# Performance work log

Hardware: AMD Instinct MI355X
Metric: run time of the kernel (lower is better)

The kernel has to match this reference:

```python
import jax, jax.numpy as jnp
import numpy as np

DIM = 128          # observed dim
LATENT = 128       # SDE state_size
HID = 128          # mu hidden width (hard-coded in source)
BROWNIAN = 2       # brownian_size
N_STEPS = 200      # Euler-Maruyama steps over t in [0, 1]
DT = 1.0 / N_STEPS


def _linear_init(key, fan_in, fan_out):
    # torch nn.Linear default: U(-1/sqrt(fan_in), 1/sqrt(fan_in))
    kw, kb = jax.random.split(key)
    bound = 1.0 / np.sqrt(fan_in)
    w = jax.random.uniform(kw, (fan_in, fan_out), jnp.float32, -bound, bound)
    b = jax.random.uniform(kb, (fan_out,), jnp.float32, -bound, bound)
    return w, b


def setup_inputs() -> dict:
    key = jax.random.key(0)
    ks = jax.random.split(key, 8)
    y = jax.random.normal(ks[0], (32768, DIM), jnp.float32)
    noise = jax.random.normal(ks[1], (N_STEPS, 32768, BROWNIAN), jnp.float32)
    enc_w, enc_b = _linear_init(ks[2], DIM, LATENT)
    mu_w1, mu_b1 = _linear_init(ks[3], LATENT, HID)
    mu_w2, mu_b2 = _linear_init(ks[4], HID, LATENT)
    sig_w, sig_b = _linear_init(ks[5], LATENT, LATENT * BROWNIAN)
    dec_w, dec_b = _linear_init(ks[6], LATENT, DIM)
    return {
        "y": y, "noise": noise,
        "enc_w": enc_w, "enc_b": enc_b,
        "mu_w1": mu_w1, "mu_b1": mu_b1, "mu_w2": mu_w2, "mu_b2": mu_b2,
        "sig_w": sig_w, "sig_b": sig_b,
        "dec_w": dec_w, "dec_b": dec_b,
    }


def reference(y, noise, enc_w, enc_b, mu_w1, mu_b1, mu_w2, mu_b2, sig_w, sig_b, dec_w, dec_b):
    B = y.shape[0]
    # encoder: Linear + exact GELU (torch nn.GELU default)
    z0 = jax.nn.gelu(y @ enc_w + enc_b, approximate=False)

    sqrt_dt = jnp.asarray(np.sqrt(DT), jnp.float32)

    def drift(z):  # f(t, y) = mu(y)
        h = jax.nn.gelu(z @ mu_w1 + mu_b1, approximate=False)
        return h @ mu_w2 + mu_b2

    def diffusion(z):  # g(t, y) -> [B, state, brownian]
        return (z @ sig_w + sig_b).reshape(B, LATENT, BROWNIAN)

    def step(z, xi):
        # Euler-Maruyama (Ito): z += f*dt + g @ dW,  dW = sqrt(dt)*xi
        dW = xi * sqrt_dt                      # [B, K]
        g = diffusion(z)                       # [B, D, K]
        z = z + drift(z) * DT + jnp.einsum("bdk,bk->bd", g, dW)
        return z, None

    zT, _ = jax.lax.scan(step, z0, noise)
    return zT @ dec_w + dec_b
```

## Files before the change

kernel.cpp:

```cpp
#include <hip/hip_runtime.h>
#include <math.h>

#define NSTEPS 200
#define NT     512
#define BR     64
#define SQDT_F 0.07071067811865475f
#define DT_F   0.005f
#define LOSCL  4096.0f
#define LOINV  2.44140625e-4f

typedef float  f32x4 __attribute__((ext_vector_type(4)));
typedef short  s16x8 __attribute__((ext_vector_type(8)));
typedef _Float16 h16x8 __attribute__((ext_vector_type(8)));
typedef unsigned short u16;
typedef unsigned short us4 __attribute__((ext_vector_type(4)));

#define ENC_OFF 0
#define W1_OFF  32768
#define W2_OFF  65536
#define WG0_OFF 98304
#define WG1_OFF 131072
#define DEC_OFF 163840
#define WPK_TOT 196608

__device__ __forceinline__ u16 f2h(float v) {
    _Float16 h = (_Float16)v;
    return __builtin_bit_cast(u16, h);
}
__device__ __forceinline__ float h2f(u16 u) {
    return (float)__builtin_bit_cast(_Float16, u);
}
__device__ __forceinline__ u16 split_hi(float v) { return f2h(v); }
__device__ __forceinline__ u16 split_lo(float v, u16 hi) {
    return f2h((v - h2f(hi)) * LOSCL);
}

__device__ __forceinline__ float gelu_fast(float x) {
    float ax = fabsf(x) * 0.70710678118654752f;
    float t  = __builtin_amdgcn_rcpf(fmaf(0.3275911f, ax, 1.0f));
    float p  = fmaf(t, 1.061405429f, -1.453152027f);
    p = fmaf(t, p, 1.421413741f);
    p = fmaf(t, p, -0.284496736f);
    p = fmaf(t, p, 0.254829592f);
    p = p * t;
    float e  = __expf(-ax * ax);
    float er = fmaf(-p, e, 1.0f);
    er = copysignf(er, x);
    return 0.5f * x * (1.0f + er);
}

__device__ __forceinline__ void mfma16(f32x4& d, s16x8 a, s16x8 b) {
    d = __builtin_amdgcn_mfma_f32_16x16x32_f16(
            __builtin_bit_cast(h16x8, a), __builtin_bit_cast(h16x8, b), d, 0, 0, 0);
}
__device__ __forceinline__ s16x8 ldf(const u16* p) {
    return *reinterpret_cast<const s16x8*>(p);
}

__device__ __forceinline__ int swz(int row) {
    return (row & 7) ^ ((row & 8) >> 2);
}

__global__ void prepack(const float* __restrict__ enc_w, const float* __restrict__ mu_w1,
                        const float* __restrict__ mu_w2, const float* __restrict__ sig_w,
                        const float* __restrict__ dec_w, u16* __restrict__ wpk)
{
    int u = blockIdx.x * 256 + threadIdx.x;
    if (u >= WPK_TOT) return;
    int mat  = u >> 15;
    int r    = u & 32767;
    int i    = r & 7;
    int lane = (r >> 3) & 63;
    int term = (r >> 9) & 1;
    int kc   = (r >> 10) & 3;
    int nt   = (r >> 12) & 7;
    int k = kc * 32 + (lane >> 4) * 8 + i;
    int n = nt * 16 + (lane & 15);
    float v;
    switch (mat) {
        case 0:  v = enc_w[k * 128 + n];         break;
        case 1:  v = mu_w1[k * 128 + n];         break;
        case 2:  v = mu_w2[k * 128 + n];         break;
        case 3:  v = sig_w[k * 256 + 2 * n];     break;
        case 4:  v = sig_w[k * 256 + 2 * n + 1]; break;
        default: v = dec_w[k * 128 + n];         break;
    }
    u16 hi = split_hi(v);
    wpk[u] = term ? split_lo(v, hi) : hi;
}

__global__ __launch_bounds__(NT) void sde_mfma(
    const float* __restrict__ y, const float* __restrict__ noise,
    const float* __restrict__ enc_b, const float* __restrict__ mu_b1,
    const float* __restrict__ mu_b2, const float* __restrict__ sig_b,
    const float* __restrict__ dec_b, const u16* __restrict__ wpk,
    float* __restrict__ out, int Btot)
{
    __shared__ __align__(16) u16 zbh[8192];
    __shared__ __align__(16) u16 zbl[8192];
    __shared__ __align__(16) u16 hbh[8192];
    __shared__ __align__(16) u16 hbl[8192];
    __shared__ float nsb[2][128];

    const int tid  = threadIdx.x;
    const int lane = tid & 63, wid = tid >> 6;
    const int ln   = lane & 15, lg = lane >> 4;
    const size_t brow = (size_t)blockIdx.x * BR;

    const int n0 = wid * 16 + ln;
    const float b10 = mu_b1[n0];
    const float b20 = mu_b2[n0];
    const float bg0 = sig_b[2 * n0];
    const float bg1 = sig_b[2 * n0 + 1];
    const int swzl = swz(ln);

    #pragma unroll
    for (int c = 0; c < 4; c++) {
        int q = c * NT + tid;
        int row = q >> 5, k4 = (q & 31) << 2;
        const float4 v = *reinterpret_cast<const float4*>(y + (brow + row) * 128 + k4);
        int idx = row * 128 + (((k4 >> 3) ^ swz(row)) << 3) + (k4 & 7);
        float vv[4] = {v.x, v.y, v.z, v.w};
        us4 hv, lv;
        #pragma unroll
        for (int e = 0; e < 4; e++) {
            u16 h = split_hi(vv[e]);
            u16 l = split_lo(vv[e], h);
            hv[e] = h; lv[e] = l;
        }
        *reinterpret_cast<us4*>(zbh + idx) = hv;
        *reinterpret_cast<us4*>(zbl + idx) = lv;
    }
    __syncthreads();

    float zr[4][4];

    {
        const float be0 = enc_b[n0];
        f32x4 a0[4], a1[4];
        #pragma unroll
        for (int mt = 0; mt < 4; mt++) {
            a0[mt] = f32x4{be0, be0, be0, be0};
            a1[mt] = f32x4{0, 0, 0, 0};
        }
        #pragma unroll
        for (int kc = 0; kc < 4; kc++) {
            int fo = (((wid << 2) | kc) << 10) + (lane << 3);
            s16x8 bh = ldf(wpk + ENC_OFF + fo);
            s16x8 bl = ldf(wpk + ENC_OFF + fo + 512);
            #pragma unroll
            for (int mt = 0; mt < 4; mt++) {
                int idx = (mt * 16 + ln) * 128 + ((((kc << 2) | lg) ^ swzl) << 3);
                s16x8 ah = ldf(zbh + idx);
                s16x8 al = ldf(zbl + idx);
                mfma16(a0[mt], ah, bh);
                mfma16(a1[mt], al, bh);
                mfma16(a1[mt], ah, bl);
            }
        }
        #pragma unroll
        for (int mt = 0; mt < 4; mt++)
            #pragma unroll
            for (int r = 0; r < 4; r++)
                zr[mt][r] = gelu_fast(fmaf(a1[mt][r], LOINV, a0[mt][r]));
    }
    __syncthreads();

    #pragma unroll
    for (int mt = 0; mt < 4; mt++)
        #pragma unroll
        for (int r = 0; r < 4; r++) {
            int m = 16 * mt + 4 * lg + r;
            int idx = m * 128 + (((n0 >> 3) ^ swz(m)) << 3) + (n0 & 7);
            u16 h = split_hi(zr[mt][r]);
            zbh[idx] = h;
            zbl[idx] = split_lo(zr[mt][r], h);
        }
    if (tid < 128) nsb[0][tid] = noise[brow * 2 + tid];
    __syncthreads();

    const u16* wq = wpk;

    for (int t = 0; t < NSTEPS; t++) {
        asm volatile("" : "+s"(wq));
        {
            int tn = (t + 1 < NSTEPS) ? (t + 1) : t;
            if (tid < 128) nsb[(t + 1) & 1][tid] = noise[((size_t)tn * Btot + brow) * 2 + tid];
        }
        {
            f32x4 a0[4], a1[4];
            #pragma unroll
            for (int mt = 0; mt < 4; mt++) {
                a0[mt] = f32x4{b10, b10, b10, b10};
                a1[mt] = f32x4{0, 0, 0, 0};
            }
            #pragma unroll
            for (int kc = 0; kc < 4; kc++) {
                int fo = (((wid << 2) | kc) << 10) + (lane << 3);
                s16x8 bh = ldf(wq + W1_OFF + fo);
                s16x8 bl = ldf(wq + W1_OFF + fo + 512);
                #pragma unroll
                for (int mt = 0; mt < 4; mt++) {
                    int idx = (mt * 16 + ln) * 128 + ((((kc << 2) | lg) ^ swzl) << 3);
                    s16x8 ah = ldf(zbh + idx);
                    s16x8 al = ldf(zbl + idx);
                    mfma16(a0[mt], ah, bh);
                    mfma16(a1[mt], al, bh);
                    mfma16(a1[mt], ah, bl);
                }
            }
            #pragma unroll
            for (int mt = 0; mt < 4; mt++)
                #pragma unroll
                for (int r = 0; r < 4; r++) {
                    float hv = gelu_fast(fmaf(a1[mt][r], LOINV, a0[mt][r]));
                    int m = 16 * mt + 4 * lg + r;
                    int idx = m * 128 + (((n0 >> 3) ^ swz(m)) << 3) + (n0 & 7);
                    u16 h = split_hi(hv);
                    hbh[idx] = h;
                    hbl[idx] = split_lo(hv, h);
                }
        }
        {
            f32x4 q0h[4], q0l[4], q1h[4], q1l[4];
            #pragma unroll
            for (int mt = 0; mt < 4; mt++) {
                q0h[mt] = f32x4{bg0, bg0, bg0, bg0}; q0l[mt] = f32x4{0, 0, 0, 0};
                q1h[mt] = f32x4{bg1, bg1, bg1, bg1}; q1l[mt] = f32x4{0, 0, 0, 0};
            }
            #pragma unroll 2
            for (int kc = 0; kc < 4; kc++) {
                int fo = (((wid << 2) | kc) << 10) + (lane << 3);
                s16x8 b0h = ldf(wq + WG0_OFF + fo);
                s16x8 b0l = ldf(wq + WG0_OFF + fo + 512);
                s16x8 b1h = ldf(wq + WG1_OFF + fo);
                s16x8 b1l = ldf(wq + WG1_OFF + fo + 512);
                #pragma unroll
                for (int mt = 0; mt < 4; mt++) {
                    int idx = (mt * 16 + ln) * 128 + ((((kc << 2) | lg) ^ swzl) << 3);
                    s16x8 ah = ldf(zbh + idx);
                    s16x8 al = ldf(zbl + idx);
                    mfma16(q0h[mt], ah, b0h);
                    mfma16(q0l[mt], al, b0h);
                    mfma16(q0l[mt], ah, b0l);
                    mfma16(q1h[mt], ah, b1h);
                    mfma16(q1l[mt], al, b1h);
                    mfma16(q1l[mt], ah, b1l);
                }
            }
            const float* np = nsb[t & 1];
            #pragma unroll
            for (int mt = 0; mt < 4; mt++)
                #pragma unroll
                for (int r = 0; r < 4; r++) {
                    int m = 16 * mt + 4 * lg + r;
                    float dw0 = np[2 * m] * SQDT_F;
                    float dw1 = np[2 * m + 1] * SQDT_F;
                    float gv0 = fmaf(q0l[mt][r], LOINV, q0h[mt][r]);
                    float gv1 = fmaf(q1l[mt][r], LOINV, q1h[mt][r]);
                    zr[mt][r] = fmaf(gv0, dw0, fmaf(gv1, dw1, zr[mt][r]));
                }
        }
        __syncthreads();

        {
            f32x4 a0[4], a1[4];
            #pragma unroll
            for (int mt = 0; mt < 4; mt++) {
                a0[mt] = f32x4{b20, b20, b20, b20};
                a1[mt] = f32x4{0, 0, 0, 0};
            }
            #pragma unroll
            for (int kc = 0; kc < 4; kc++) {
                int fo = (((wid << 2) | kc) << 10) + (lane << 3);
                s16x8 bh = ldf(wq + W2_OFF + fo);
                s16x8 bl = ldf(wq + W2_OFF + fo + 512);
                #pragma unroll
                for (int mt = 0; mt < 4; mt++) {
                    int idx = (mt * 16 + ln) * 128 + ((((kc << 2) | lg) ^ swzl) << 3);
                    s16x8 ah = ldf(hbh + idx);
                    s16x8 al = ldf(hbl + idx);
                    mfma16(a0[mt], ah, bh);
                    mfma16(a1[mt], al, bh);
                    mfma16(a1[mt], ah, bl);
                }
            }
            #pragma unroll
            for (int mt = 0; mt < 4; mt++)
                #pragma unroll
                for (int r = 0; r < 4; r++) {
                    float drift = fmaf(a1[mt][r], LOINV, a0[mt][r]);
                    float v = fmaf(drift, DT_F, zr[mt][r]);
                    zr[mt][r] = v;
                    int m = 16 * mt + 4 * lg + r;
                    int idx = m * 128 + (((n0 >> 3) ^ swz(m)) << 3) + (n0 & 7);
                    u16 h = split_hi(v);
                    zbh[idx] = h;
                    zbl[idx] = split_lo(v, h);
                }
        }
        __syncthreads();
    }

    {
        const float bd0 = dec_b[n0];
        f32x4 a0[4], a1[4];
        #pragma unroll
        for (int mt = 0; mt < 4; mt++) {
            a0[mt] = f32x4{bd0, bd0, bd0, bd0};
            a1[mt] = f32x4{0, 0, 0, 0};
        }
        #pragma unroll
        for (int kc = 0; kc < 4; kc++) {
            int fo = (((wid << 2) | kc) << 10) + (lane << 3);
            s16x8 bh = ldf(wpk + DEC_OFF + fo);
            s16x8 bl = ldf(wpk + DEC_OFF + fo + 512);
            #pragma unroll
            for (int mt = 0; mt < 4; mt++) {
                int idx = (mt * 16 + ln) * 128 + ((((kc << 2) | lg) ^ swzl) << 3);
                s16x8 ah = ldf(zbh + idx);
                s16x8 al = ldf(zbl + idx);
                mfma16(a0[mt], ah, bh);
                mfma16(a1[mt], al, bh);
                mfma16(a1[mt], ah, bl);
            }
        }
        #pragma unroll
        for (int mt = 0; mt < 4; mt++)
            #pragma unroll
            for (int r = 0; r < 4; r++) {
                int m = 16 * mt + 4 * lg + r;
                out[(brow + m) * 128 + n0] = fmaf(a1[mt][r], LOINV, a0[mt][r]);
            }
    }
}

extern "C" void kernel_launch(void* const* d_in, const int* in_sizes, int n_in,
                              void* d_out, int out_size, void* d_ws, size_t ws_size,
                              hipStream_t stream) {
    const float* y     = (const float*)d_in[0];
    const float* noise = (const float*)d_in[1];
    const float* enc_w = (const float*)d_in[2];
    const float* enc_b = (const float*)d_in[3];
    const float* mu_w1 = (const float*)d_in[4];
    const float* mu_b1 = (const float*)d_in[5];
    const float* mu_w2 = (const float*)d_in[6];
    const float* mu_b2 = (const float*)d_in[7];
    const float* sig_w = (const float*)d_in[8];
    const float* sig_b = (const float*)d_in[9];
    const float* dec_w = (const float*)d_in[10];
    const float* dec_b = (const float*)d_in[11];
    float* out = (float*)d_out;
    u16* wpk = (u16*)d_ws;

    const int Btot = in_sizes[0] / 128;
    prepack<<<(WPK_TOT + 255) / 256, 256, 0, stream>>>(enc_w, mu_w1, mu_w2, sig_w, dec_w, wpk);
    sde_mfma<<<Btot / BR, NT, 0, stream>>>(y, noise, enc_b, mu_b1, mu_b2, sig_b, dec_b,
                                           wpk, out, Btot);
}
```

Baseline: 2.877 ms.

## Transpose MFMA roles so weights are A operand, shrink block to 16 rows

Restructures the SDE kernel so each block handles 16 batch rows with 256 threads instead of 64 rows with 512. Weights become the MFMA A operand and activations the B operand, with a new k-permuted prepack. Each wave owns two output 16-column tiles, and activations pass through small register-fragment-shaped LDS buffers (double-buffered z) rather than swizzled full-row tiles. The aim is more blocks for better occupancy and latency hiding, and less LDS traffic per step, at the cost of reloading weight fragments from global/L2 for four times as many blocks.

```diff
diff --git a/kernel.cpp b/kernel.cpp
--- a/kernel.cpp
+++ b/kernel.cpp
@@ -2,8 +2,8 @@
 #include <math.h>
 
 #define NSTEPS 200
-#define NT     512
-#define BR     64
+#define NT     256
+#define BR     16
 #define SQDT_F 0.07071067811865475f
 #define DT_F   0.005f
 #define LOSCL  4096.0f
@@ -13,7 +13,6 @@
 typedef short  s16x8 __attribute__((ext_vector_type(8)));
 typedef _Float16 h16x8 __attribute__((ext_vector_type(8)));
 typedef unsigned short u16;
-typedef unsigned short us4 __attribute__((ext_vector_type(4)));
 
 #define ENC_OFF 0
 #define W1_OFF  32768
@@ -55,10 +54,6 @@
 }
 __device__ __forceinline__ s16x8 ldf(const u16* p) {
     return *reinterpret_cast<const s16x8*>(p);
-}
-
-__device__ __forceinline__ int swz(int row) {
-    return (row & 7) ^ ((row & 8) >> 2);
 }
 
 __global__ void prepack(const float* __restrict__ enc_w, const float* __restrict__ mu_w1,
@@ -74,7 +69,7 @@
     int term = (r >> 9) & 1;
     int kc   = (r >> 10) & 3;
     int nt   = (r >> 12) & 7;
-    int k = kc * 32 + (lane >> 4) * 8 + i;
+    int k = kc * 32 + 16 * (i >> 2) + 4 * (lane >> 4) + (i & 3);
     int n = nt * 16 + (lane & 15);
     float v;
     switch (mat) {
@@ -96,87 +91,66 @@
     const float* __restrict__ dec_b, const u16* __restrict__ wpk,
     float* __restrict__ out, int Btot)
 {
-    __shared__ __align__(16) u16 zbh[8192];
-    __shared__ __align__(16) u16 zbl[8192];
-    __shared__ __align__(16) u16 hbh[8192];
-    __shared__ __align__(16) u16 hbl[8192];
-    __shared__ float nsb[2][128];
+    __shared__ __align__(16) u16 zx[2][4][2][512];
+    __shared__ __align__(16) u16 hx[4][2][512];
+    __shared__ float bb[4][128];
+    __shared__ float nsb[2][32];
 
     const int tid  = threadIdx.x;
     const int lane = tid & 63, wid = tid >> 6;
     const int ln   = lane & 15, lg = lane >> 4;
     const size_t brow = (size_t)blockIdx.x * BR;
 
-    const int n0 = wid * 16 + ln;
-    const float b10 = mu_b1[n0];
-    const float b20 = mu_b2[n0];
-    const float bg0 = sig_b[2 * n0];
-    const float bg1 = sig_b[2 * n0 + 1];
-    const int swzl = swz(ln);
-
-    #pragma unroll
-    for (int c = 0; c < 4; c++) {
-        int q = c * NT + tid;
-        int row = q >> 5, k4 = (q & 31) << 2;
-        const float4 v = *reinterpret_cast<const float4*>(y + (brow + row) * 128 + k4);
-        int idx = row * 128 + (((k4 >> 3) ^ swz(row)) << 3) + (k4 & 7);
-        float vv[4] = {v.x, v.y, v.z, v.w};
-        us4 hv, lv;
-        #pragma unroll
-        for (int e = 0; e < 4; e++) {
-            u16 h = split_hi(vv[e]);
-            u16 l = split_lo(vv[e], h);
-            hv[e] = h; lv[e] = l;
-        }
-        *reinterpret_cast<us4*>(zbh + idx) = hv;
-        *reinterpret_cast<us4*>(zbl + idx) = lv;
-    }
-    __syncthreads();
-
-    float zr[4][4];
+    if (tid < 128) {
+        bb[0][tid] = mu_b1[tid];
+        bb[1][tid] = mu_b2[tid];
+        bb[2][tid] = sig_b[2 * tid];
+        bb[3][tid] = sig_b[2 * tid + 1];
+    }
+    if (tid < 32) nsb[0][tid] = noise[(brow + (tid >> 1)) * 2 + (tid & 1)];
+    volatile const float (*bbv)[128] = (volatile const float (*)[128])bb;
+
+    float zm[2][4];
 
     {
-        const float be0 = enc_b[n0];
-        f32x4 a0[4], a1[4];
-        #pragma unroll
-        for (int mt = 0; mt < 4; mt++) {
-            a0[mt] = f32x4{be0, be0, be0, be0};
-            a1[mt] = f32x4{0, 0, 0, 0};
-        }
+        s16x8 yfh[4], yfl[4];
         #pragma unroll
         for (int kc = 0; kc < 4; kc++) {
-            int fo = (((wid << 2) | kc) << 10) + (lane << 3);
-            s16x8 bh = ldf(wpk + ENC_OFF + fo);
-            s16x8 bl = ldf(wpk + ENC_OFF + fo + 512);
-            #pragma unroll
-            for (int mt = 0; mt < 4; mt++) {
-                int idx = (mt * 16 + ln) * 128 + ((((kc << 2) | lg) ^ swzl) << 3);
-                s16x8 ah = ldf(zbh + idx);
-                s16x8 al = ldf(zbl + idx);
-                mfma16(a0[mt], ah, bh);
-                mfma16(a1[mt], al, bh);
-                mfma16(a1[mt], ah, bl);
-            }
-        }
-        #pragma unroll
-        for (int mt = 0; mt < 4; mt++)
+            float vv[8];
+            #pragma unroll
+            for (int s = 0; s < 2; s++) {
+                const float4 v = *reinterpret_cast<const float4*>(
+                    y + (brow + ln) * 128 + kc * 32 + 16 * s + 4 * lg);
+                vv[4*s+0] = v.x; vv[4*s+1] = v.y; vv[4*s+2] = v.z; vv[4*s+3] = v.w;
+            }
+            s16x8 th, tl;
+            #pragma unroll
+            for (int e = 0; e < 8; e++) {
+                u16 hh = split_hi(vv[e]);
+                th[e] = (short)hh;
+                tl[e] = (short)split_lo(vv[e], hh);
+            }
+            yfh[kc] = th; yfl[kc] = tl;
+        }
+        #pragma unroll
+        for (int s = 0; s < 2; s++) {
+            const int jt = 2 * wid + s;
+            f32x4 a0, a1;
+            #pragma unroll
+            for (int r = 0; r < 4; r++) { a0[r] = enc_b[16 * jt + 4 * lg + r]; a1[r] = 0.0f; }
+            #pragma unroll
+            for (int kc = 0; kc < 4; kc++) {
+                const u16* ap = wpk + ENC_OFF + ((jt * 4 + kc) * 2) * 512 + lane * 8;
+                s16x8 wh = ldf(ap), wl = ldf(ap + 512);
+                mfma16(a0, wh, yfh[kc]);
+                mfma16(a1, wl, yfh[kc]);
+                mfma16(a1, wh, yfl[kc]);
+            }
             #pragma unroll
             for (int r = 0; r < 4; r++)
-                zr[mt][r] = gelu_fast(fmaf(a1[mt][r], LOINV, a0[mt][r]));
-    }
-    __syncthreads();
-
-    #pragma unroll
-    for (int mt = 0; mt < 4; mt++)
-        #pragma unroll
-        for (int r = 0; r < 4; r++) {
-            int m = 16 * mt + 4 * lg + r;
-            int idx = m * 128 + (((n0 >> 3) ^ swz(m)) << 3) + (n0 & 7);
-            u16 h = split_hi(zr[mt][r]);
-            zbh[idx] = h;
-            zbl[idx] = split_lo(zr[mt][r], h);
-        }
-    if (tid < 128) nsb[0][tid] = noise[brow * 2 + tid];
+                zm[s][r] = gelu_fast(fmaf(a1[r], LOINV, a0[r]));
+        }
+    }
     __syncthreads();
 
     const u16* wq = wpk;
@@ -185,153 +159,163 @@
         asm volatile("" : "+s"(wq));
         {
             int tn = (t + 1 < NSTEPS) ? (t + 1) : t;
-            if (tid < 128) nsb[(t + 1) & 1][tid] = noise[((size_t)tn * Btot + brow) * 2 + tid];
-        }
-        {
-            f32x4 a0[4], a1[4];
-            #pragma unroll
-            for (int mt = 0; mt < 4; mt++) {
-                a0[mt] = f32x4{b10, b10, b10, b10};
-                a1[mt] = f32x4{0, 0, 0, 0};
-            }
+            if (tid < 32)
+                nsb[(t + 1) & 1][tid] = noise[((size_t)tn * Btot + brow + (tid >> 1)) * 2 + (tid & 1)];
+        }
+        {
+            s16x8 th, tl;
+            #pragma unroll
+            for (int e = 0; e < 8; e++) {
+                float v = zm[e >> 2][e & 3];
+                u16 hh = split_hi(v);
+                th[e] = (short)hh;
+                tl[e] = (short)split_lo(v, hh);
+            }
+            *reinterpret_cast<s16x8*>(&zx[t & 1][wid][0][lane * 8]) = th;
+            *reinterpret_cast<s16x8*>(&zx[t & 1][wid][1][lane * 8]) = tl;
+        }
+        __syncthreads();
+
+        s16x8 zfh[4], zfl[4];
+        #pragma unroll
+        for (int kc = 0; kc < 4; kc++) {
+            zfh[kc] = ldf(&zx[t & 1][kc][0][lane * 8]);
+            zfl[kc] = ldf(&zx[t & 1][kc][1][lane * 8]);
+        }
+
+        float hvv[2][4];
+        #pragma unroll
+        for (int s = 0; s < 2; s++) {
+            const int jt = 2 * wid + s;
+            f32x4 a0, a1;
+            #pragma unroll
+            for (int r = 0; r < 4; r++) { a0[r] = bbv[0][16 * jt + 4 * lg + r]; a1[r] = 0.0f; }
             #pragma unroll
             for (int kc = 0; kc < 4; kc++) {
-                int fo = (((wid << 2) | kc) << 10) + (lane << 3);
-                s16x8 bh = ldf(wq + W1_OFF + fo);
-                s16x8 bl = ldf(wq + W1_OFF + fo + 512);
-                #pragma unroll
-                for (int mt = 0; mt < 4; mt++) {
-                    int idx = (mt * 16 + ln) * 128 + ((((kc << 2) | lg) ^ swzl) << 3);
-                    s16x8 ah = ldf(zbh + idx);
-                    s16x8 al = ldf(zbl + idx);
-                    mfma16(a0[mt], ah, bh);
-                    mfma16(a1[mt], al, bh);
-                    mfma16(a1[mt], ah, bl);
+                const u16* ap = wq + W1_OFF + ((jt * 4 + kc) * 2) * 512 + lane * 8;
+                s16x8 wh = ldf(ap), wl = ldf(ap + 512);
+                mfma16(a0, wh, zfh[kc]);
+                mfma16(a1, wl, zfh[kc]);
+                mfma16(a1, wh, zfl[kc]);
+            }
+            #pragma unroll
+            for (int r = 0; r < 4; r++)
+                hvv[s][r] = gelu_fast(fmaf(a1[r], LOINV, a0[r]));
+        }
+        {
+            s16x8 th, tl;
+            #pragma unroll
+            for (int e = 0; e < 8; e++) {
+                float v = hvv[e >> 2][e & 3];
+                u16 hh = split_hi(v);
+                th[e] = (short)hh;
+                tl[e] = (short)split_lo(v, hh);
+            }
+            *reinterpret_cast<s16x8*>(&hx[wid][0][lane * 8]) = th;
+            *reinterpret_cast<s16x8*>(&hx[wid][1][lane * 8]) = tl;
+        }
+
+        {
+            const float dw0 = nsb[t & 1][2 * ln] * SQDT_F;
+            const float dw1 = nsb[t & 1][2 * ln + 1] * SQDT_F;
+            #pragma unroll
+            for (int s = 0; s < 2; s++) {
+                const int nt = 2 * wid + s;
+                f32x4 q0h, q0l, q1h, q1l;
+                #pragma unroll
+                for (int r = 0; r < 4; r++) {
+                    q0h[r] = bbv[2][16 * nt + 4 * lg + r]; q0l[r] = 0.0f;
+                    q1h[r] = bbv[3][16 * nt + 4 * lg + r]; q1l[r] = 0.0f;
                 }
-            }
-            #pragma unroll
-            for (int mt = 0; mt < 4; mt++)
+                #pragma unroll
+                for (int kc = 0; kc < 4; kc++) {
+                    const u16* p0 = wq + WG0_OFF + ((nt * 4 + kc) * 2) * 512 + lane * 8;
+                    const u16* p1 = wq + WG1_OFF + ((nt * 4 + kc) * 2) * 512 + lane * 8;
+                    s16x8 w0h = ldf(p0), w0l = ldf(p0 + 512);
+                    s16x8 w1h = ldf(p1), w1l = ldf(p1 + 512);
+                    mfma16(q0h, w0h, zfh[kc]);
+                    mfma16(q0l, w0l, zfh[kc]);
+                    mfma16(q0l, w0h, zfl[kc]);
+                    mfma16(q1h, w1h, zfh[kc]);
+                    mfma16(q1l, w1l, zfh[kc]);
+                    mfma16(q1l, w1h, zfl[kc]);
+                }
                 #pragma unroll
                 for (int r = 0; r < 4; r++) {
-                    float hv = gelu_fast(fmaf(a1[mt][r], LOINV, a0[mt][r]));
-                    int m = 16 * mt + 4 * lg + r;
-                    int idx = m * 128 + (((n0 >> 3) ^ swz(m)) << 3) + (n0 & 7);
-                    u16 h = split_hi(hv);
-                    hbh[idx] = h;
-                    hbl[idx] = split_lo(hv, h);
+                    float gv0 = fmaf(q0l[r], LOINV, q0h[r]);
+                    float gv1 = fmaf(q1l[r], LOINV, q1h[r]);
+                    zm[s][r] = fmaf(gv0, dw0, fmaf(gv1, dw1, zm[s][r]));
                 }
-        }
-        {
-            f32x4 q0h[4], q0l[4], q1h[4], q1l[4];
-            #pragma unroll
-            for (int mt = 0; mt < 4; mt++) {
-                q0h[mt] = f32x4{bg0, bg0, bg0, bg0}; q0l[mt] = f32x4{0, 0, 0, 0};
-                q1h[mt] = f32x4{bg1, bg1, bg1, bg1}; q1l[mt] = f32x4{0, 0, 0, 0};
-            }
-            #pragma unroll 2
+            }
+        }
+        __syncthreads();
+
+        {
+            s16x8 hfh[4], hfl[4];
+            #pragma unroll
             for (int kc = 0; kc < 4; kc++) {
-                int fo = (((wid << 2) | kc) << 10) + (lane << 3);
-                s16x8 b0h = ldf(wq + WG0_OFF + fo);
-                s16x8 b0l = ldf(wq + WG0_OFF + fo + 512);
-                s16x8 b1h = ldf(wq + WG1_OFF + fo);
-                s16x8 b1l = ldf(wq + WG1_OFF + fo + 512);
-                #pragma unroll
-                for (int mt = 0; mt < 4; mt++) {
-                    int idx = (mt * 16 + ln) * 128 + ((((kc << 2) | lg) ^ swzl) << 3);
-                    s16x8 ah = ldf(zbh + idx);
-                    s16x8 al = ldf(zbl + idx);
-                    mfma16(q0h[mt], ah, b0h);
-                    mfma16(q0l[mt], al, b0h);
-                    mfma16(q0l[mt], ah, b0l);
-                    mfma16(q1h[mt], ah, b1h);
-                    mfma16(q1l[mt], al, b1h);
-                    mfma16(q1l[mt], ah, b1l);
+                hfh[kc] = ldf(&hx[kc][0][lane * 8]);
+                hfl[kc] = ldf(&hx[kc][1][lane * 8]);
+            }
+            #pragma unroll
+            for (int s = 0; s < 2; s++) {
+                const int nt = 2 * wid + s;
+                f32x4 a0, a1;
+                #pragma unroll
+                for (int r = 0; r < 4; r++) { a0[r] = bbv[1][16 * nt + 4 * lg + r]; a1[r] = 0.0f; }
+                #pragma unroll
+                for (int kc = 0; kc < 4; kc++) {
+                    const u16* ap = wq + W2_OFF + ((nt * 4 + kc) * 2) * 512 + lane * 8;
+                    s16x8 wh = ldf(ap), wl = ldf(ap + 512);
+                    mfma16(a0, wh, hfh[kc]);
+                    mfma16(a1, wl, hfh[kc]);
+                    mfma16(a1, wh, hfl[kc]);
                 }
-            }
-            const float* np = nsb[t & 1];
-            #pragma unroll
-            for (int mt = 0; mt < 4; mt++)
-                #pragma unroll
-                for (int r = 0; r < 4; r++) {
-                    int m = 16 * mt + 4 * lg + r;
-                    float dw0 = np[2 * m] * SQDT_F;
-                    float dw1 = np[2 * m + 1] * SQDT_F;
-                    float gv0 = fmaf(q0l[mt][r], LOINV, q0h[mt][r]);
-                    float gv1 = fmaf(q1l[mt][r], LOINV, q1h[mt][r]);
-                    zr[mt][r] = fmaf(gv0, dw0, fmaf(gv1, dw1, zr[mt][r]));
-                }
-        }
-        __syncthreads();
-
-        {
-            f32x4 a0[4], a1[4];
-            #pragma unroll
-            for (int mt = 0; mt < 4; mt++) {
-                a0[mt] = f32x4{b20, b20, b20, b20};
-                a1[mt] = f32x4{0, 0, 0, 0};
-            }
+                #pragma unroll
+                for (int r = 0; r < 4; r++)
+                    zm[s][r] = fmaf(fmaf(a1[r], LOINV, a0[r]), DT_F, zm[s][r]);
+            }
+        }
+    }
+
+    {
+        s16x8 th, tl;
+        #pragma unroll
+        for (int e = 0; e < 8; e++) {
+            float v = zm[e >> 2][e & 3];
+            u16 hh = split_hi(v);
+            th[e] = (short)hh;
+            tl[e] = (short)split_lo(v, hh);
+        }
+        *reinterpret_cast<s16x8*>(&zx[0][wid][0][lane * 8]) = th;
+        *reinterpret_cast<s16x8*>(&zx[0][wid][1][lane * 8]) = tl;
+    }
+    __syncthreads();
+    {
+        s16x8 zfh[4], zfl[4];
+        #pragma unroll
+        for (int kc = 0; kc < 4; kc++) {
+            zfh[kc] = ldf(&zx[0][kc][0][lane * 8]);
+            zfl[kc] = ldf(&zx[0][kc][1][lane * 8]);
+        }
+        #pragma unroll
+        for (int s = 0; s < 2; s++) {
+            const int nt = 2 * wid + s;
+            f32x4 a0, a1;
+            #pragma unroll
+            for (int r = 0; r < 4; r++) { a0[r] = dec_b[16 * nt + 4 * lg + r]; a1[r] = 0.0f; }
             #pragma unroll
             for (int kc = 0; kc < 4; kc++) {
-                int fo = (((wid << 2) | kc) << 10) + (lane << 3);
-                s16x8 bh = ldf(wq + W2_OFF + fo);
-                s16x8 bl = ldf(wq + W2_OFF + fo + 512);
-                #pragma unroll
-                for (int mt = 0; mt < 4; mt++) {
-                    int idx = (mt * 16 + ln) * 128 + ((((kc << 2) | lg) ^ swzl) << 3);
-                    s16x8 ah = ldf(hbh + idx);
-                    s16x8 al = ldf(hbl + idx);
-                    mfma16(a0[mt], ah, bh);
-                    mfma16(a1[mt], al, bh);
-                    mfma16(a1[mt], ah, bl);
-                }
-            }
-            #pragma unroll
-            for (int mt = 0; mt < 4; mt++)
-                #pragma unroll
-                for (int r = 0; r < 4; r++) {
-                    float drift = fmaf(a1[mt][r], LOINV, a0[mt][r]);
-                    float v = fmaf(drift, DT_F, zr[mt][r]);
-                    zr[mt][r] = v;
-                    int m = 16 * mt + 4 * lg + r;
-                    int idx = m * 128 + (((n0 >> 3) ^ swz(m)) << 3) + (n0 & 7);
-                    u16 h = split_hi(v);
-                    zbh[idx] = h;
-                    zbl[idx] = split_lo(v, h);
-                }
-        }
-        __syncthreads();
-    }
-
-    {
-        const float bd0 = dec_b[n0];
-        f32x4 a0[4], a1[4];
-        #pragma unroll
-        for (int mt = 0; mt < 4; mt++) {
-            a0[mt] = f32x4{bd0, bd0, bd0, bd0};
-            a1[mt] = f32x4{0, 0, 0, 0};
-        }
-        #pragma unroll
-        for (int kc = 0; kc < 4; kc++) {
-            int fo = (((wid << 2) | kc) << 10) + (lane << 3);
-            s16x8 bh = ldf(wpk + DEC_OFF + fo);
-            s16x8 bl = ldf(wpk + DEC_OFF + fo + 512);
-            #pragma unroll
-            for (int mt = 0; mt < 4; mt++) {
-                int idx = (mt * 16 + ln) * 128 + ((((kc << 2) | lg) ^ swzl) << 3);
-                s16x8 ah = ldf(zbh + idx);
-                s16x8 al = ldf(zbl + idx);
-                mfma16(a0[mt], ah, bh);
-                mfma16(a1[mt], al, bh);
-                mfma16(a1[mt], ah, bl);
-            }
-        }
-        #pragma unroll
-        for (int mt = 0; mt < 4; mt++)
-            #pragma unroll
-            for (int r = 0; r < 4; r++) {
-                int m = 16 * mt + 4 * lg + r;
-                out[(brow + m) * 128 + n0] = fmaf(a1[mt][r], LOINV, a0[mt][r]);
-            }
+                const u16* ap = wpk + DEC_OFF + ((nt * 4 + kc) * 2) * 512 + lane * 8;
+                s16x8 wh = ldf(ap), wl = ldf(ap + 512);
+                mfma16(a0, wh, zfh[kc]);
+                mfma16(a1, wl, zfh[kc]);
+                mfma16(a1, wh, zfl[kc]);
+            }
+            #pragma unroll
+            for (int r = 0; r < 4; r++)
+                out[(brow + ln) * 128 + 16 * nt + 4 * lg + r] = fmaf(a1[r], LOINV, a0[r]);
+        }
     }
 }
 
```

New measurement: 5.220 ms. 81.5% more time.

## Pack two independent 64-row groups into one 1024-thread block

Applied to the files above, without the earlier changes.

Each block now runs two independent 512-thread halves, each handling its own 64 batch rows with separate LDS buffers, so a block covers 128 rows and the grid is halved. Both halves share __syncthreads, which could let weight fetches from global/L2 be shared or cached across the pair and changes how waves are scheduled per CU. The cost is twice the LDS per block (about 128KB) and block-wide barriers that couple two independent problems, which may limit occupancy and add barrier stalls.

```diff
diff --git a/kernel.cpp b/kernel.cpp
--- a/kernel.cpp
+++ b/kernel.cpp
@@ -2,8 +2,8 @@
 #include <math.h>
 
 #define NSTEPS 200
-#define NT     512
-#define BR     64
+#define NT     1024
+#define BRB    128
 #define SQDT_F 0.07071067811865475f
 #define DT_F   0.005f
 #define LOSCL  4096.0f
@@ -96,16 +96,18 @@
     const float* __restrict__ dec_b, const u16* __restrict__ wpk,
     float* __restrict__ out, int Btot)
 {
-    __shared__ __align__(16) u16 zbh[8192];
-    __shared__ __align__(16) u16 zbl[8192];
-    __shared__ __align__(16) u16 hbh[8192];
-    __shared__ __align__(16) u16 hbl[8192];
-    __shared__ float nsb[2][128];
+    __shared__ __align__(16) u16 zbh[2][8192];
+    __shared__ __align__(16) u16 zbl[2][8192];
+    __shared__ __align__(16) u16 hbh[2][8192];
+    __shared__ __align__(16) u16 hbl[2][8192];
+    __shared__ float nsb[2][2][128];
 
     const int tid  = threadIdx.x;
-    const int lane = tid & 63, wid = tid >> 6;
+    const int pid  = tid >> 9;
+    const int ptid = tid & 511;
+    const int lane = ptid & 63, wid = ptid >> 6;
     const int ln   = lane & 15, lg = lane >> 4;
-    const size_t brow = (size_t)blockIdx.x * BR;
+    const size_t brow = (size_t)blockIdx.x * BRB + (size_t)pid * 64;
 
     const int n0 = wid * 16 + ln;
     const float b10 = mu_b1[n0];
@@ -116,7 +118,7 @@
 
     #pragma unroll
     for (int c = 0; c < 4; c++) {
-        int q = c * NT + tid;
+        int q = c * 512 + ptid;
         int row = q >> 5, k4 = (q & 31) << 2;
         const float4 v = *reinterpret_cast<const float4*>(y + (brow + row) * 128 + k4);
         int idx = row * 128 + (((k4 >> 3) ^ swz(row)) << 3) + (k4 & 7);
@@ -128,8 +130,8 @@
             u16 l = split_lo(vv[e], h);
             hv[e] = h; lv[e] = l;
         }
-        *reinterpret_cast<us4*>(zbh + idx) = hv;
-        *reinterpret_cast<us4*>(zbl + idx) = lv;
+        *reinterpret_cast<us4*>(&zbh[pid][idx]) = hv;
+        *reinterpret_cast<us4*>(&zbl[pid][idx]) = lv;
     }
     __syncthreads();
 
@@ -151,8 +153,8 @@
             #pragma unroll
             for (int mt = 0; mt < 4; mt++) {
                 int idx = (mt * 16 + ln) * 128 + ((((kc << 2) | lg) ^ swzl) << 3);
-                s16x8 ah = ldf(zbh + idx);
-                s16x8 al = ldf(zbl + idx);
+                s16x8 ah = ldf(&zbh[pid][idx]);
+                s16x8 al = ldf(&zbl[pid][idx]);
                 mfma16(a0[mt], ah, bh);
                 mfma16(a1[mt], al, bh);
                 mfma16(a1[mt], ah, bl);
@@ -173,10 +175,10 @@
             int m = 16 * mt + 4 * lg + r;
             int idx = m * 128 + (((n0 >> 3) ^ swz(m)) << 3) + (n0 & 7);
             u16 h = split_hi(zr[mt][r]);
-            zbh[idx] = h;
-            zbl[idx] = split_lo(zr[mt][r], h);
-        }
-    if (tid < 128) nsb[0][tid] = noise[brow * 2 + tid];
+            zbh[pid][idx] = h;
+            zbl[pid][idx] = split_lo(zr[mt][r], h);
+        }
+    if (ptid < 128) nsb[pid][0][ptid] = noise[brow * 2 + ptid];
     __syncthreads();
 
     const u16* wq = wpk;
@@ -185,7 +187,7 @@
         asm volatile("" : "+s"(wq));
         {
             int tn = (t + 1 < NSTEPS) ? (t + 1) : t;
-            if (tid < 128) nsb[(t + 1) & 1][tid] = noise[((size_t)tn * Btot + brow) * 2 + tid];
+            if (ptid < 128) nsb[pid][(t + 1) & 1][ptid] = noise[((size_t)tn * Btot + brow) * 2 + ptid];
         }
         {
             f32x4 a0[4], a1[4];
@@ -202,8 +204,8 @@
                 #pragma unroll
                 for (int mt = 0; mt < 4; mt++) {
                     int idx = (mt * 16 + ln) * 128 + ((((kc << 2) | lg) ^ swzl) << 3);
-                    s16x8 ah = ldf(zbh + idx);
-                    s16x8 al = ldf(zbl + idx);
+                    s16x8 ah = ldf(&zbh[pid][idx]);
+                    s16x8 al = ldf(&zbl[pid][idx]);
                     mfma16(a0[mt], ah, bh);
                     mfma16(a1[mt], al, bh);
                     mfma16(a1[mt], ah, bl);
@@ -217,8 +219,8 @@
                     int m = 16 * mt + 4 * lg + r;
                     int idx = m * 128 + (((n0 >> 3) ^ swz(m)) << 3) + (n0 & 7);
                     u16 h = split_hi(hv);
-                    hbh[idx] = h;
-                    hbl[idx] = split_lo(hv, h);
+                    hbh[pid][idx] = h;
+                    hbl[pid][idx] = split_lo(hv, h);
                 }
         }
         {
@@ -238,8 +240,8 @@
                 #pragma unroll
                 for (int mt = 0; mt < 4; mt++) {
                     int idx = (mt * 16 + ln) * 128 + ((((kc << 2) | lg) ^ swzl) << 3);
-                    s16x8 ah = ldf(zbh + idx);
-                    s16x8 al = ldf(zbl + idx);
+                    s16x8 ah = ldf(&zbh[pid][idx]);
+                    s16x8 al = ldf(&zbl[pid][idx]);
                     mfma16(q0h[mt], ah, b0h);
                     mfma16(q0l[mt], al, b0h);
                     mfma16(q0l[mt], ah, b0l);
@@ -248,7 +250,7 @@
                     mfma16(q1l[mt], ah, b1l);
                 }
             }
-            const float* np = nsb[t & 1];
+            const float* np = nsb[pid][t & 1];
             #pragma unroll
             for (int mt = 0; mt < 4; mt++)
                 #pragma unroll
@@ -278,8 +280,8 @@
                 #pragma unroll
                 for (int mt = 0; mt < 4; mt++) {
                     int idx = (mt * 16 + ln) * 128 + ((((kc << 2) | lg) ^ swzl) << 3);
-                    s16x8 ah = ldf(hbh + idx);
-                    s16x8 al = ldf(hbl + idx);
+                    s16x8 ah = ldf(&hbh[pid][idx]);
+                    s16x8 al = ldf(&hbl[pid][idx]);
                     mfma16(a0[mt], ah, bh);
                     mfma16(a1[mt], al, bh);
                     mfma16(a1[mt], ah, bl);
@@ -295,8 +297,8 @@
                     int m = 16 * mt + 4 * lg + r;
                     int idx = m * 128 + (((n0 >> 3) ^ swz(m)) << 3) + (n0 & 7);
                     u16 h = split_hi(v);
-                    zbh[idx] = h;
-                    zbl[idx] = split_lo(v, h);
+                    zbh[pid][idx] = h;
+                    zbl[pid][idx] = split_lo(v, h);
                 }
         }
         __syncthreads();
@@ -318,8 +320,8 @@
             #pragma unroll
             for (int mt = 0; mt < 4; mt++) {
                 int idx = (mt * 16 + ln) * 128 + ((((kc << 2) | lg) ^ swzl) << 3);
-                s16x8 ah = ldf(zbh + idx);
-                s16x8 al = ldf(zbl + idx);
+                s16x8 ah = ldf(&zbh[pid][idx]);
+                s16x8 al = ldf(&zbl[pid][idx]);
                 mfma16(a0[mt], ah, bh);
                 mfma16(a1[mt], al, bh);
                 mfma16(a1[mt], ah, bl);
@@ -355,6 +357,6 @@
 
     const int Btot = in_sizes[0] / 128;
     prepack<<<(WPK_TOT + 255) / 256, 256, 0, stream>>>(enc_w, mu_w1, mu_w2, sig_w, dec_w, wpk);
-    sde_mfma<<<Btot / BR, NT, 0, stream>>>(y, noise, enc_b, mu_b1, mu_b2, sig_b, dec_b,
-                                           wpk, out, Btot);
-}
+    sde_mfma<<<Btot / BRB, NT, 0, stream>>>(y, noise, enc_b, mu_b1, mu_b2, sig_b, dec_b,
+                                            wpk, out, Btot);
+}
```

Result: slower. 5.469 ms (+90.1%).

## Transpose MFMA operand roles and repack activations into fragment-native LDS layout

Applied to the files above, without the earlier changes.

Swaps the MFMA operands so weights act as the A operand and activations as B, producing outputs where each lane holds four consecutive features of one row. Activations are stored in LDS in the exact fragment order the MFMA reads, with hi/lo halves interleaved, replacing the XOR-swizzled row-major layout and scalar 16-bit stores with vectorized 4-element stores. The weight prepack permutes the k index to match. Biases move to shared memory read through volatile loads, the output store becomes a float4 write, and noise is indexed per row. This is meant to cut LDS store instructions and address arithmetic, at the cost of possible new bank conflicts and extra LDS bias reads.

```diff
diff --git a/kernel.cpp b/kernel.cpp
--- a/kernel.cpp
+++ b/kernel.cpp
@@ -22,6 +22,8 @@
 #define WG1_OFF 131072
 #define DEC_OFF 163840
 #define WPK_TOT 196608
+
+#define FO(kc, mt, term) (((((kc) * 4 + (mt)) * 2) + (term)) * 512)
 
 __device__ __forceinline__ u16 f2h(float v) {
     _Float16 h = (_Float16)v;
@@ -55,10 +57,6 @@
 }
 __device__ __forceinline__ s16x8 ldf(const u16* p) {
     return *reinterpret_cast<const s16x8*>(p);
-}
-
-__device__ __forceinline__ int swz(int row) {
-    return (row & 7) ^ ((row & 8) >> 2);
 }
 
 __global__ void prepack(const float* __restrict__ enc_w, const float* __restrict__ mu_w1,
@@ -74,7 +72,7 @@
     int term = (r >> 9) & 1;
     int kc   = (r >> 10) & 3;
     int nt   = (r >> 12) & 7;
-    int k = kc * 32 + (lane >> 4) * 8 + i;
+    int k = kc * 32 + 16 * (i >> 2) + 4 * (lane >> 4) + (i & 3);
     int n = nt * 16 + (lane & 15);
     float v;
     switch (mat) {
@@ -96,86 +94,86 @@
     const float* __restrict__ dec_b, const u16* __restrict__ wpk,
     float* __restrict__ out, int Btot)
 {
-    __shared__ __align__(16) u16 zbh[8192];
-    __shared__ __align__(16) u16 zbl[8192];
-    __shared__ __align__(16) u16 hbh[8192];
-    __shared__ __align__(16) u16 hbl[8192];
+    __shared__ __align__(16) u16 zx[16384];
+    __shared__ __align__(16) u16 hx[16384];
+    __shared__ float bb[4][128];
     __shared__ float nsb[2][128];
 
     const int tid  = threadIdx.x;
-    const int lane = tid & 63, wid = tid >> 6;
+    const int lane = tid & 63, jt = tid >> 6;
     const int ln   = lane & 15, lg = lane >> 4;
     const size_t brow = (size_t)blockIdx.x * BR;
 
-    const int n0 = wid * 16 + ln;
-    const float b10 = mu_b1[n0];
-    const float b20 = mu_b2[n0];
-    const float bg0 = sig_b[2 * n0];
-    const float bg1 = sig_b[2 * n0 + 1];
-    const int swzl = swz(ln);
+    const int jb  = 16 * jt + 4 * lg;
+    const int pub = FO(jt >> 1, 0, 0) + lane * 8 + 4 * (jt & 1);
+
+    if (tid < 128)      bb[0][tid]       = mu_b1[tid];
+    else if (tid < 256) bb[1][tid - 128] = mu_b2[tid - 128];
+    else if (tid < 384) bb[2][tid - 256] = sig_b[2 * (tid - 256)];
+    else                bb[3][tid - 384] = sig_b[2 * (tid - 384) + 1];
+    volatile const float* vb = &bb[0][0];
 
     #pragma unroll
-    for (int c = 0; c < 4; c++) {
-        int q = c * NT + tid;
-        int row = q >> 5, k4 = (q & 31) << 2;
-        const float4 v = *reinterpret_cast<const float4*>(y + (brow + row) * 128 + k4);
-        int idx = row * 128 + (((k4 >> 3) ^ swz(row)) << 3) + (k4 & 7);
+    for (int cc = 0; cc < 4; cc++) {
+        int q = cc * NT + tid;
+        int m = q >> 5, cq = (q & 31) << 2;
+        const float4 v = *reinterpret_cast<const float4*>(y + (brow + m) * 128 + cq);
+        int kc = cq >> 5, a = (cq >> 4) & 1, b = (cq >> 2) & 3;
+        int ad = FO(kc, m >> 4, 0) + ((m & 15) + 16 * b) * 8 + 4 * a;
         float vv[4] = {v.x, v.y, v.z, v.w};
         us4 hv, lv;
         #pragma unroll
         for (int e = 0; e < 4; e++) {
             u16 h = split_hi(vv[e]);
-            u16 l = split_lo(vv[e], h);
-            hv[e] = h; lv[e] = l;
-        }
-        *reinterpret_cast<us4*>(zbh + idx) = hv;
-        *reinterpret_cast<us4*>(zbl + idx) = lv;
+            hv[e] = h; lv[e] = split_lo(vv[e], h);
+        }
+        *reinterpret_cast<us4*>(zx + ad)       = hv;
+        *reinterpret_cast<us4*>(zx + ad + 512) = lv;
     }
     __syncthreads();
 
-    float zr[4][4];
+    float zm[4][4];
 
     {
-        const float be0 = enc_b[n0];
+        f32x4 eb;
+        #pragma unroll
+        for (int r = 0; r < 4; r++) eb[r] = enc_b[jb + r];
         f32x4 a0[4], a1[4];
         #pragma unroll
-        for (int mt = 0; mt < 4; mt++) {
-            a0[mt] = f32x4{be0, be0, be0, be0};
-            a1[mt] = f32x4{0, 0, 0, 0};
-        }
-        #pragma unroll
+        for (int mt = 0; mt < 4; mt++) { a0[mt] = eb; a1[mt] = f32x4{0, 0, 0, 0}; }
+        #pragma unroll 2
         for (int kc = 0; kc < 4; kc++) {
-            int fo = (((wid << 2) | kc) << 10) + (lane << 3);
-            s16x8 bh = ldf(wpk + ENC_OFF + fo);
-            s16x8 bl = ldf(wpk + ENC_OFF + fo + 512);
-            #pragma unroll
-            for (int mt = 0; mt < 4; mt++) {
-                int idx = (mt * 16 + ln) * 128 + ((((kc << 2) | lg) ^ swzl) << 3);
-                s16x8 ah = ldf(zbh + idx);
-                s16x8 al = ldf(zbl + idx);
-                mfma16(a0[mt], ah, bh);
-                mfma16(a1[mt], al, bh);
-                mfma16(a1[mt], ah, bl);
+            const u16* ap = wpk + ENC_OFF + ((jt * 4 + kc) * 2) * 512 + lane * 8;
+            s16x8 wh = ldf(ap), wl = ldf(ap + 512);
+            #pragma unroll
+            for (int mt = 0; mt < 4; mt++) {
+                int zo = FO(kc, mt, 0) + lane * 8;
+                s16x8 zh_ = ldf(zx + zo), zl_ = ldf(zx + zo + 512);
+                mfma16(a0[mt], wh, zh_);
+                mfma16(a1[mt], wl, zh_);
+                mfma16(a1[mt], wh, zl_);
             }
         }
         #pragma unroll
         for (int mt = 0; mt < 4; mt++)
             #pragma unroll
             for (int r = 0; r < 4; r++)
-                zr[mt][r] = gelu_fast(fmaf(a1[mt][r], LOINV, a0[mt][r]));
+                zm[mt][r] = gelu_fast(fmaf(a1[mt][r], LOINV, a0[mt][r]));
     }
     __syncthreads();
 
     #pragma unroll
-    for (int mt = 0; mt < 4; mt++)
+    for (int mt = 0; mt < 4; mt++) {
+        us4 hv, lv;
         #pragma unroll
         for (int r = 0; r < 4; r++) {
-            int m = 16 * mt + 4 * lg + r;
-            int idx = m * 128 + (((n0 >> 3) ^ swz(m)) << 3) + (n0 & 7);
-            u16 h = split_hi(zr[mt][r]);
-            zbh[idx] = h;
-            zbl[idx] = split_lo(zr[mt][r], h);
-        }
+            u16 h = split_hi(zm[mt][r]);
+            hv[r] = h; lv[r] = split_lo(zm[mt][r], h);
+        }
+        int ad = pub + mt * 1024;
+        *reinterpret_cast<us4*>(zx + ad)       = hv;
+        *reinterpret_cast<us4*>(zx + ad + 512) = lv;
+    }
     if (tid < 128) nsb[0][tid] = noise[brow * 2 + tid];
     __syncthreads();
 
@@ -188,150 +186,152 @@
             if (tid < 128) nsb[(t + 1) & 1][tid] = noise[((size_t)tn * Btot + brow) * 2 + tid];
         }
         {
+            f32x4 b1v;
+            #pragma unroll
+            for (int r = 0; r < 4; r++) b1v[r] = vb[0 * 128 + jb + r];
             f32x4 a0[4], a1[4];
             #pragma unroll
-            for (int mt = 0; mt < 4; mt++) {
-                a0[mt] = f32x4{b10, b10, b10, b10};
-                a1[mt] = f32x4{0, 0, 0, 0};
-            }
-            #pragma unroll
-            for (int kc = 0; kc < 4; kc++) {
-                int fo = (((wid << 2) | kc) << 10) + (lane << 3);
-                s16x8 bh = ldf(wq + W1_OFF + fo);
-                s16x8 bl = ldf(wq + W1_OFF + fo + 512);
-                #pragma unroll
-                for (int mt = 0; mt < 4; mt++) {
-                    int idx = (mt * 16 + ln) * 128 + ((((kc << 2) | lg) ^ swzl) << 3);
-                    s16x8 ah = ldf(zbh + idx);
-                    s16x8 al = ldf(zbl + idx);
-                    mfma16(a0[mt], ah, bh);
-                    mfma16(a1[mt], al, bh);
-                    mfma16(a1[mt], ah, bl);
-                }
-            }
-            #pragma unroll
-            for (int mt = 0; mt < 4; mt++)
-                #pragma unroll
-                for (int r = 0; r < 4; r++) {
-                    float hv = gelu_fast(fmaf(a1[mt][r], LOINV, a0[mt][r]));
-                    int m = 16 * mt + 4 * lg + r;
-                    int idx = m * 128 + (((n0 >> 3) ^ swz(m)) << 3) + (n0 & 7);
-                    u16 h = split_hi(hv);
-                    hbh[idx] = h;
-                    hbl[idx] = split_lo(hv, h);
-                }
-        }
-        {
-            f32x4 q0h[4], q0l[4], q1h[4], q1l[4];
-            #pragma unroll
-            for (int mt = 0; mt < 4; mt++) {
-                q0h[mt] = f32x4{bg0, bg0, bg0, bg0}; q0l[mt] = f32x4{0, 0, 0, 0};
-                q1h[mt] = f32x4{bg1, bg1, bg1, bg1}; q1l[mt] = f32x4{0, 0, 0, 0};
-            }
+            for (int mt = 0; mt < 4; mt++) { a0[mt] = b1v; a1[mt] = f32x4{0, 0, 0, 0}; }
             #pragma unroll 2
             for (int kc = 0; kc < 4; kc++) {
-                int fo = (((wid << 2) | kc) << 10) + (lane << 3);
-                s16x8 b0h = ldf(wq + WG0_OFF + fo);
-                s16x8 b0l = ldf(wq + WG0_OFF + fo + 512);
-                s16x8 b1h = ldf(wq + WG1_OFF + fo);
-                s16x8 b1l = ldf(wq + WG1_OFF + fo + 512);
+                const u16* ap = wq + W1_OFF + ((jt * 4 + kc) * 2) * 512 + lane * 8;
+                s16x8 wh = ldf(ap), wl = ldf(ap + 512);
                 #pragma unroll
                 for (int mt = 0; mt < 4; mt++) {
-                    int idx = (mt * 16 + ln) * 128 + ((((kc << 2) | lg) ^ swzl) << 3);
-                    s16x8 ah = ldf(zbh + idx);
-                    s16x8 al = ldf(zbl + idx);
-                    mfma16(q0h[mt], ah, b0h);
-                    mfma16(q0l[mt], al, b0h);
-                    mfma16(q0l[mt], ah, b0l);
-                    mfma16(q1h[mt], ah, b1h);
-                    mfma16(q1l[mt], al, b1h);
-                    mfma16(q1l[mt], ah, b1l);
+                    int zo = FO(kc, mt, 0) + lane * 8;
+                    s16x8 zh_ = ldf(zx + zo), zl_ = ldf(zx + zo + 512);
+                    mfma16(a0[mt], wh, zh_);
+                    mfma16(a1[mt], wl, zh_);
+                    mfma16(a1[mt], wh, zl_);
+                }
+            }
+            #pragma unroll
+            for (int mt = 0; mt < 4; mt++) {
+                us4 hv, lv;
+                #pragma unroll
+                for (int r = 0; r < 4; r++) {
+                    float h = gelu_fast(fmaf(a1[mt][r], LOINV, a0[mt][r]));
+                    u16 hh = split_hi(h);
+                    hv[r] = hh; lv[r] = split_lo(h, hh);
+                }
+                int ad = pub + mt * 1024;
+                *reinterpret_cast<us4*>(hx + ad)       = hv;
+                *reinterpret_cast<us4*>(hx + ad + 512) = lv;
+            }
+        }
+        {
+            f32x4 g0v, g1v;
+            #pragma unroll
+            for (int r = 0; r < 4; r++) {
+                g0v[r] = vb[2 * 128 + jb + r];
+                g1v[r] = vb[3 * 128 + jb + r];
+            }
+            f32x4 q0h[4], q0l[4], q1h[4], q1l[4];
+            #pragma unroll
+            for (int mt = 0; mt < 4; mt++) {
+                q0h[mt] = g0v; q0l[mt] = f32x4{0, 0, 0, 0};
+                q1h[mt] = g1v; q1l[mt] = f32x4{0, 0, 0, 0};
+            }
+            #pragma unroll 2
+            for (int kc = 0; kc < 4; kc++) {
+                const u16* p0 = wq + WG0_OFF + ((jt * 4 + kc) * 2) * 512 + lane * 8;
+                const u16* p1 = wq + WG1_OFF + ((jt * 4 + kc) * 2) * 512 + lane * 8;
+                s16x8 w0h = ldf(p0), w0l = ldf(p0 + 512);
+                s16x8 w1h = ldf(p1), w1l = ldf(p1 + 512);
+                #pragma unroll
+                for (int mt = 0; mt < 4; mt++) {
+                    int zo = FO(kc, mt, 0) + lane * 8;
+                    s16x8 zh_ = ldf(zx + zo), zl_ = ldf(zx + zo + 512);
+                    mfma16(q0h[mt], w0h, zh_);
+                    mfma16(q0l[mt], w0l, zh_);
+                    mfma16(q0l[mt], w0h, zl_);
+                    mfma16(q1h[mt], w1h, zh_);
+                    mfma16(q1l[mt], w1l, zh_);
+                    mfma16(q1l[mt], w1h, zl_);
                 }
             }
             const float* np = nsb[t & 1];
             #pragma unroll
-            for (int mt = 0; mt < 4; mt++)
+            for (int mt = 0; mt < 4; mt++) {
+                int mrow = ln + 16 * mt;
+                float dw0 = np[2 * mrow] * SQDT_F;
+                float dw1 = np[2 * mrow + 1] * SQDT_F;
                 #pragma unroll
                 for (int r = 0; r < 4; r++) {
-                    int m = 16 * mt + 4 * lg + r;
-                    float dw0 = np[2 * m] * SQDT_F;
-                    float dw1 = np[2 * m + 1] * SQDT_F;
                     float gv0 = fmaf(q0l[mt][r], LOINV, q0h[mt][r]);
                     float gv1 = fmaf(q1l[mt][r], LOINV, q1h[mt][r]);
-                    zr[mt][r] = fmaf(gv0, dw0, fmaf(gv1, dw1, zr[mt][r]));
-                }
+                    zm[mt][r] = fmaf(gv0, dw0, fmaf(gv1, dw1, zm[mt][r]));
+                }
+            }
         }
         __syncthreads();
 
         {
+            f32x4 b2v;
+            #pragma unroll
+            for (int r = 0; r < 4; r++) b2v[r] = vb[1 * 128 + jb + r];
             f32x4 a0[4], a1[4];
             #pragma unroll
-            for (int mt = 0; mt < 4; mt++) {
-                a0[mt] = f32x4{b20, b20, b20, b20};
-                a1[mt] = f32x4{0, 0, 0, 0};
-            }
-            #pragma unroll
+            for (int mt = 0; mt < 4; mt++) { a0[mt] = b2v; a1[mt] = f32x4{0, 0, 0, 0}; }
+            #pragma unroll 2
             for (int kc = 0; kc < 4; kc++) {
-                int fo = (((wid << 2) | kc) << 10) + (lane << 3);
-                s16x8 bh = ldf(wq + W2_OFF + fo);
-                s16x8 bl = ldf(wq + W2_OFF + fo + 512);
+                const u16* ap = wq + W2_OFF + ((jt * 4 + kc) * 2) * 512 + lane * 8;
+                s16x8 wh = ldf(ap), wl = ldf(ap + 512);
                 #pragma unroll
                 for (int mt = 0; mt < 4; mt++) {
-                    int idx = (mt * 16 + ln) * 128 + ((((kc << 2) | lg) ^ swzl) << 3);
-                    s16x8 ah = ldf(hbh + idx);
-                    s16x8 al = ldf(hbl + idx);
-                    mfma16(a0[mt], ah, bh);
-                    mfma16(a1[mt], al, bh);
-                    mfma16(a1[mt], ah, bl);
-                }
-            }
-            #pragma unroll
-            for (int mt = 0; mt < 4; mt++)
+                    int ho = FO(kc, mt, 0) + lane * 8;
+                    s16x8 hh_ = ldf(hx + ho), hl_ = ldf(hx + ho + 512);
+                    mfma16(a0[mt], wh, hh_);
+                    mfma16(a1[mt], wl, hh_);
+                    mfma16(a1[mt], wh, hl_);
+                }
+            }
+            #pragma unroll
+            for (int mt = 0; mt < 4; mt++) {
+                us4 hv, lv;
                 #pragma unroll
                 for (int r = 0; r < 4; r++) {
                     float drift = fmaf(a1[mt][r], LOINV, a0[mt][r]);
-                    float v = fmaf(drift, DT_F, zr[mt][r]);
-                    zr[mt][r] = v;
-                    int m = 16 * mt + 4 * lg + r;
-                    int idx = m * 128 + (((n0 >> 3) ^ swz(m)) << 3) + (n0 & 7);
-                    u16 h = split_hi(v);
-                    zbh[idx] = h;
-                    zbl[idx] = split_lo(v, h);
-                }
+                    float v = fmaf(drift, DT_F, zm[mt][r]);
+                    zm[mt][r] = v;
+                    u16 hh = split_hi(v);
+                    hv[r] = hh; lv[r] = split_lo(v, hh);
+                }
+                int ad = pub + mt * 1024;
+                *reinterpret_cast<us4*>(zx + ad)       = hv;
+                *reinterpret_cast<us4*>(zx + ad + 512) = lv;
+            }
         }
         __syncthreads();
     }
 
     {
-        const float bd0 = dec_b[n0];
+        f32x4 dbv;
+        #pragma unroll
+        for (int r = 0; r < 4; r++) dbv[r] = dec_b[jb + r];
         f32x4 a0[4], a1[4];
         #pragma unroll
+        for (int mt = 0; mt < 4; mt++) { a0[mt] = dbv; a1[mt] = f32x4{0, 0, 0, 0}; }
+        #pragma unroll 2
+        for (int kc = 0; kc < 4; kc++) {
+            const u16* ap = wpk + DEC_OFF + ((jt * 4 + kc) * 2) * 512 + lane * 8;
+            s16x8 wh = ldf(ap), wl = ldf(ap + 512);
+            #pragma unroll
+            for (int mt = 0; mt < 4; mt++) {
+                int zo = FO(kc, mt, 0) + lane * 8;
+                s16x8 zh_ = ldf(zx + zo), zl_ = ldf(zx + zo + 512);
+                mfma16(a0[mt], wh, zh_);
+                mfma16(a1[mt], wl, zh_);
+                mfma16(a1[mt], wh, zl_);
+            }
+        }
+        #pragma unroll
         for (int mt = 0; mt < 4; mt++) {
-            a0[mt] = f32x4{bd0, bd0, bd0, bd0};
-            a1[mt] = f32x4{0, 0, 0, 0};
-        }
-        #pragma unroll
-        for (int kc = 0; kc < 4; kc++) {
-            int fo = (((wid << 2) | kc) << 10) + (lane << 3);
-            s16x8 bh = ldf(wpk + DEC_OFF + fo);
-            s16x8 bl = ldf(wpk + DEC_OFF + fo + 512);
-            #pragma unroll
-            for (int mt = 0; mt < 4; mt++) {
-                int idx = (mt * 16 + ln) * 128 + ((((kc << 2) | lg) ^ swzl) << 3);
-                s16x8 ah = ldf(zbh + idx);
-                s16x8 al = ldf(zbl + idx);
-                mfma16(a0[mt], ah, bh);
-                mfma16(a1[mt], al, bh);
-                mfma16(a1[mt], ah, bl);
-            }
-        }
-        #pragma unroll
-        for (int mt = 0; mt < 4; mt++)
-            #pragma unroll
-            for (int r = 0; r < 4; r++) {
-                int m = 16 * mt + 4 * lg + r;
-                out[(brow + m) * 128 + n0] = fmaf(a1[mt][r], LOINV, a0[mt][r]);
-            }
+            f32x4 o;
+            #pragma unroll
+            for (int r = 0; r < 4; r++) o[r] = fmaf(a1[mt][r], LOINV, a0[mt][r]);
+            *reinterpret_cast<f32x4*>(out + (brow + ln + 16 * mt) * 128 + jb) = o;
+        }
     }
 }
 
```

Measured after the change: 2.738 ms (median of 2 runs). -4.8%, faster.
